# Optimization experiments

Measured on AMD Instinct MI355X. Metric: run time of the kernel, lower is better.

## Reference

```python
import jax, jax.numpy as jnp
import numpy as np
from math import factorial as fac

LMAX = 3
NMAX = 3
RC = 6.0
UNIT = RC / 3.0  # atomic_unit = rc/3
NSPEC = 4
N_ATOMS = 1000000


def _nnl():
    # a_{n,l} = 1 / ((2l+1) * 2^(2n+l) * n! * (n+l)!); nnl = sqrt(a_n a_n')
    a = np.array([[1.0 / ((2 * l + 1) * 2 ** (2 * n + l) * fac(n) * fac(n + l))
                   for l in range(LMAX + 1)] for n in range(NMAX + 1)])
    return jnp.asarray(np.sqrt(a[None] * a[:, None]), jnp.float32)  # (n, n', L+1)


def _yr_yi():
    one = np.ones((LMAX + 1, LMAX + 1))
    Yr = 2 * np.tril(one) - np.eye(LMAX + 1)   # real parts: diag weight 1 (m=0), lower weight 2
    Yi = 2 * np.triu(one, 1)                   # imag parts: strict upper weight 2
    return jnp.asarray(Yr, jnp.float32), jnp.asarray(Yi, jnp.float32)


def _sh_single(v):
    # Solid harmonics r^l * Ylm for one atom, packed into a (L+1, L+1) matrix:
    # Re(Y_l^m) at [l, l-m] (m=0 on the diagonal), Im(Y_l^m) at [l-m, l].
    x, y, z = v[0], v[1], v[2]
    r2 = x * x + y * y + z * z
    re = {(0, 0): jnp.asarray(0.28209479177387814, v.dtype)}  # 1/sqrt(4*pi)
    im = {(0, 0): jnp.zeros((), v.dtype)}
    for l in range(1, LMAX + 1):
        cl = -float(np.sqrt((2 * l + 1) / (2.0 * l)))
        re[(l, l)] = cl * (x * re[(l - 1, l - 1)] - y * im[(l - 1, l - 1)])
        im[(l, l)] = cl * (x * im[(l - 1, l - 1)] + y * re[(l - 1, l - 1)])
        g = float(np.sqrt(2 * l + 1))
        re[(l, l - 1)] = g * z * re[(l - 1, l - 1)]
        im[(l, l - 1)] = g * z * im[(l - 1, l - 1)]
        for m in range(l - 1):
            a = float(np.sqrt((4 * l * l - 1) / (l * l - m * m)))
            b = float(np.sqrt(((l - 1) ** 2 - m * m) / (4.0 * (l - 1) ** 2 - 1)))
            re[(l, m)] = a * (z * re[(l - 1, m)] - b * r2 * re[(l - 2, m)])
            im[(l, m)] = a * (z * im[(l - 1, m)] - b * r2 * im[(l - 2, m)])
    Y = jnp.zeros((LMAX + 1, LMAX + 1), v.dtype)
    for l in range(LMAX + 1):
        for m in range(l + 1):
            Y = Y.at[l, l - m].set(re[(l, m)])
            if m > 0:
                Y = Y.at[l - m, l].set(im[(l, m)])
    return Y


def _radial(dist):
    # Exp(-0.5 d^2/unit^2) * PolyCut(rc): smooth radial with polynomial cutoff
    cut = jnp.where(dist < RC, (1.0 - dist / RC) ** 2, 0.0)
    return jnp.exp(-0.5 * dist * dist / (UNIT * UNIT)) * cut


def _forward(coo, numbers):
    xyz = coo / UNIT
    d = jnp.sqrt(jnp.sum(xyz * xyz, axis=-1))              # (N,)
    n = 2.0 * jnp.arange(NMAX + 1, dtype=coo.dtype)        # exponents 2n
    r = _radial(UNIT * d)                                   # (N,)
    f = r[None] * d[None] ** n[:, None]                     # (nmax+1, N)
    Y = jnp.moveaxis(jax.vmap(_sh_single)(xyz), 0, -1)      # (L+1, L+1, N)
    onehot = (numbers[None, :] == jnp.arange(NSPEC)[:, None]).astype(coo.dtype)  # (S, N)
    # species-grouped reduction of the radial x Ylm outer product (fused einsum)
    c = jnp.einsum('kn,abn,sn->skab', f, Y, onehot)         # (S, nmax+1, L+1, L+1)
    Yr, Yi = _yr_yi()
    # p[a,b,n,m,l] = sum_m' Re-part + Im-part of c_{b,m} c*_{a,n} power spectrum
    p1 = jnp.einsum('bmlj,anlj,lj->abnml', c, c, Yr)
    p2 = jnp.einsum('bmil,anil,il->abnml', c, c, Yi)
    p = (p1 + p2) * _nnl()[None, None]
    return p.reshape(-1)                                    # dim = S^2 (nmax+1)^2 (L+1) = 1024


def setup_inputs() -> dict:
    key = jax.random.key(0)
    k1, k2 = jax.random.split(key)
    coo = 3.0 * jax.random.normal(k1, (N_ATOMS, 3), dtype=jnp.float32)
    numbers = jax.random.randint(k2, (N_ATOMS,), 0, NSPEC)
    return {"coo": coo, "numbers": numbers}


def reference(coo, numbers):
    return _forward(coo, numbers)
```

## Files before the change

### kernel.cpp

```cpp
#include <hip/hip_runtime.h>
#include <hip/hip_bf16.h>
#include <hip/hip_fp16.h>


typedef float f32x4 __attribute__((ext_vector_type(4)));
typedef unsigned int uint4v __attribute__((ext_vector_type(4)));
typedef _Float16 h2 __attribute__((ext_vector_type(2)));
typedef _Float16 half8 __attribute__((ext_vector_type(8)));

#define NB 512
#define NCH 4

__global__ void __launch_bounds__(256) soap_accum(
    const float* __restrict__ coo, const int* __restrict__ numbers,
    int N, float* __restrict__ partials, float* __restrict__ c_ws,
    int* __restrict__ counter)
{
    __shared__ unsigned int lT[4][2][16][64];

    if (blockIdx.x == 0) {
        if (threadIdx.x < 256) c_ws[threadIdx.x] = 0.f;
        if (threadIdx.x == 0) *counter = 0;
    }

    const int lane = threadIdx.x & 63;
    const int w = threadIdx.x >> 6;
    const int g = lane >> 4;
    const int comp = lane & 15;

    unsigned int* lA = &lT[w][0][0][0];
    unsigned int* lB = &lT[w][1][0][0];

    const unsigned swz = (unsigned)((comp & 7) << 2);
    const unsigned rbase = (unsigned)(comp << 6);
    unsigned rd[4];
#pragma unroll
    for (int m = 0; m < 4; ++m)
        rd[m] = rbase + ((unsigned)(16 * m + 4 * g) ^ swz);

    f32x4 acc = {0.f, 0.f, 0.f, 0.f};

    const int wid = blockIdx.x * 4 + w;
    float X0[NCH], Y0[NCH], Z0[NCH], X1[NCH], Y1[NCH], Z1[NCH];
    int n0[NCH], n1[NCH];
#pragma unroll
    for (int k = 0; k < NCH; ++k) {
        int base = (wid + k * 2048) * 128;
        int p = base + 2 * lane;
        int pc = p < N - 1 ? p : N - 2;
        const float* cb = coo + 3 * pc;
        float2 c0 = *(const float2*)(cb);
        float2 c1 = *(const float2*)(cb + 2);
        float2 c2 = *(const float2*)(cb + 4);
        X0[k] = c0.x; Y0[k] = c0.y; Z0[k] = c1.x;
        X1[k] = c1.y; Y1[k] = c2.x; Z1[k] = c2.y;
        int2 nm = *(const int2*)(numbers + pc);
        n0[k] = p < N ? nm.x : -1;
        n1[k] = p + 1 < N ? nm.y : -1;
    }

#pragma unroll
    for (int k = 0; k < NCH; ++k) {
        int num0 = n0[k], num1 = n1[k];

        float x0 = X0[k] * 0.5f, y0 = Y0[k] * 0.5f, z0 = Z0[k] * 0.5f;
        float x1 = X1[k] * 0.5f, y1 = Y1[k] * 0.5f, z1 = Z1[k] * 0.5f;
        float r20 = x0 * x0 + y0 * y0 + z0 * z0;
        float r21 = x1 * x1 + y1 * y1 + z1 * z1;
        float t0 = fmaxf(1.f - sqrtf(r20) * (1.f / 3.f), 0.f);
        float t1 = fmaxf(1.f - sqrtf(r21) * (1.f / 3.f), 0.f);
        float f00 = __expf(-0.5f * r20) * t0 * t0;
        float f01 = __expf(-0.5f * r21) * t1 * t1;

        h2 fpk[4];
        fpk[0] = (h2){(_Float16)f00, (_Float16)f01};
        fpk[1] = (h2){(_Float16)(f00 * r20), (_Float16)(f01 * r21)};
        fpk[2] = (h2){(_Float16)(f00 * r20 * r20), (_Float16)(f01 * r21 * r21)};
        fpk[3] = (h2){(_Float16)(f00 * r20 * r20 * r20), (_Float16)(f01 * r21 * r21 * r21)};

        h2 msk[4];
#pragma unroll
        for (int s = 0; s < 4; ++s)
            msk[s] = (h2){(_Float16)(num0 == s ? 1.f : 0.f),
                          (_Float16)(num1 == s ? 1.f : 0.f)};

        h2 xp = (h2){(_Float16)x0, (_Float16)x1};
        h2 yp = (h2){(_Float16)y0, (_Float16)y1};
        h2 zp = (h2){(_Float16)z0, (_Float16)z1};
        h2 rp = (h2){(_Float16)r20, (_Float16)r21};

        h2 re11 = (_Float16)-0.34549414947133550f * xp;
        h2 im11 = (_Float16)-0.34549414947133550f * yp;
        h2 re10 = (_Float16) 0.48860251190291992f * zp;
        h2 re22 = (_Float16)-1.11803398874989490f * (xp * re11 - yp * im11);
        h2 im22 = (_Float16)-1.11803398874989490f * (xp * im11 + yp * re11);
        h2 re21 = (_Float16) 2.23606797749978970f * (zp * re11);
        h2 im21 = (_Float16) 2.23606797749978970f * (zp * im11);
        h2 re20 = (_Float16) 1.93649167310370850f * (zp * re10 - (_Float16)0.16286750396763996f * rp);
        h2 re33 = (_Float16)-1.08012344973464350f * (xp * re22 - yp * im22);
        h2 im33 = (_Float16)-1.08012344973464350f * (xp * im22 + yp * re22);
        h2 re32 = (_Float16) 2.64575131106459070f * (zp * re22);
        h2 im32 = (_Float16) 2.64575131106459070f * (zp * im22);
        h2 re31 = (_Float16) 2.09165006633518890f * (zp * re21 - (_Float16)0.44721359549995793f * (rp * re11));
        h2 im31 = (_Float16) 2.09165006633518890f * (zp * im21 - (_Float16)0.44721359549995793f * (rp * im11));
        h2 re30 = (_Float16) 1.97202659436653870f * (zp * re20 - (_Float16)0.51639777949432220f * (rp * re10));

        h2 ypk[16];
        ypk[0] = (h2){(_Float16)0.28209479177387814f, (_Float16)0.28209479177387814f};
        ypk[1] = im11; ypk[2]  = im22; ypk[3]  = im33;
        ypk[4] = re11; ypk[5]  = re10; ypk[6]  = im21; ypk[7]  = im32;
        ypk[8] = re22; ypk[9]  = re21; ypk[10] = re20; ypk[11] = im31;
        ypk[12] = re33; ypk[13] = re32; ypk[14] = re31; ypk[15] = re30;

#pragma unroll
        for (int c = 0; c < 16; ++c) {
            h2 fs = fpk[c & 3] * msk[c >> 2];
            union { h2 h; unsigned u; } ua, ub;
            ua.h = fs; ub.h = ypk[c];
            unsigned idx = (unsigned)(c << 6) + ((unsigned)lane ^ ((unsigned)(c & 7) << 2));
            lA[idx] = ua.u;
            lB[idx] = ub.u;
        }

#pragma unroll
        for (int m = 0; m < 4; ++m) {
            union { uint4v q; half8 h; } A, B;
            A.q = *(const uint4v*)&lA[rd[m]];
            B.q = *(const uint4v*)&lB[rd[m]];
            acc = __builtin_amdgcn_mfma_f32_16x16x32_f16(A.h, B.h, acc, 0, 0, 0);
        }
    }

    float* credw = (float*)&lT[w][0][0][0];
#pragma unroll
    for (int rr = 0; rr < 4; ++rr)
        credw[((lane >> 4) * 4 + rr) * 16 + (lane & 15)] = acc[rr];
    __syncthreads();

    int tt = threadIdx.x;
    partials[blockIdx.x * 256 + tt] =
        ((float*)&lT[0][0][0][0])[tt] + ((float*)&lT[1][0][0][0])[tt] +
        ((float*)&lT[2][0][0][0])[tt] + ((float*)&lT[3][0][0][0])[tt];
}

__global__ void __launch_bounds__(256) soap_reduce_final(
    const float* __restrict__ partials, float* __restrict__ c_ws,
    int* __restrict__ counter, float* __restrict__ out)
{
    __shared__ float cs[256];
    __shared__ int lastflag;
    int t = threadIdx.x;

    float v = 0.f;
    for (int r = blockIdx.x; r < NB; r += 32)
        v += partials[r * 256 + t];
    atomicAdd(&c_ws[t], v);
    __syncthreads();
    if (t == 0) {
        __threadfence();
        lastflag = (atomicAdd(counter, 1) == 31);
    }
    __syncthreads();
    if (!lastflag) return;

    __threadfence();
    cs[t] = __hip_atomic_load(&c_ws[t], __ATOMIC_RELAXED,
                              __HIP_MEMORY_SCOPE_AGENT);
    __syncthreads();

    const float fact[7] = {1.f, 1.f, 2.f, 6.f, 24.f, 120.f, 720.f};
#pragma unroll
    for (int k = 0; k < 4; ++k) {
        int o = k * 256 + t;
        int l = o & 3, m = (o >> 2) & 3, n = (o >> 4) & 3,
            b = (o >> 6) & 3, a = (o >> 8) & 3;
        const float* cbm = &cs[(b * 4 + m) * 16];
        const float* can = &cs[(a * 4 + n) * 16];
        float vv = 0.f;
        for (int j = 0; j <= l; ++j) {
            float wgt = (j == l) ? 1.f : 2.f;
            vv += wgt * cbm[l * 4 + j] * can[l * 4 + j];
        }
        for (int i = 0; i < l; ++i)
            vv += 2.f * cbm[i * 4 + l] * can[i * 4 + l];
        float an = 1.0f / ((float)(2 * l + 1) * (float)(1 << (2 * n + l)) * fact[n] * fact[n + l]);
        float am = 1.0f / ((float)(2 * l + 1) * (float)(1 << (2 * m + l)) * fact[m] * fact[m + l]);
        out[o] = vv * sqrtf(an * am);
    }
}

extern "C" void kernel_launch(void* const* d_in, const int* in_sizes, int n_in,
                              void* d_out, int out_size, void* d_ws, size_t ws_size,
                              hipStream_t stream)
{
    const float* coo = (const float*)d_in[0];
    const int* numbers = (const int*)d_in[1];
    int N = in_sizes[1];

    float* c_ws = (float*)d_ws;
    int* counter = (int*)((float*)d_ws + 256);
    float* partials = (float*)d_ws + 512;

    hipLaunchKernelGGL(soap_accum, dim3(NB), dim3(256), 0, stream,
                       coo, numbers, N, partials, c_ws, counter);
    hipLaunchKernelGGL(soap_reduce_final, dim3(32), dim3(256), 0, stream,
                       partials, c_ws, counter, (float*)d_out);
}
```

Baseline: 17.28 us.

## Fuse reduction into accumulation kernel via two-level last-block counters

Drops the separate reduce kernel. Each block now writes its partial, and the last block in each group of 16 (found with an atomic counter) sums that group. The last of 32 group reducers then computes the final power spectrum. This removes a kernel launch and the gap between launches. Counters are never reset; they depend on modulo wraparound and on the workspace being zeroed at first use.

After: 54.98 us. 218% more time.

```diff
diff --git a/kernel.cpp b/kernel.cpp
--- a/kernel.cpp
+++ b/kernel.cpp
@@ -11,17 +11,14 @@
 #define NB 512
 #define NCH 4
 
-__global__ void __launch_bounds__(256) soap_accum(
+__global__ void __launch_bounds__(256) soap_fused(
     const float* __restrict__ coo, const int* __restrict__ numbers,
-    int N, float* __restrict__ partials, float* __restrict__ c_ws,
-    int* __restrict__ counter)
+    int N, float* __restrict__ partials, float* __restrict__ gsum,
+    unsigned* __restrict__ gcnt, float* __restrict__ out)
 {
     __shared__ unsigned int lT[4][2][16][64];
-
-    if (blockIdx.x == 0) {
-        if (threadIdx.x < 256) c_ws[threadIdx.x] = 0.f;
-        if (threadIdx.x == 0) *counter = 0;
-    }
+    __shared__ float cs[256];
+    __shared__ int flag1, flag2;
 
     const int lane = threadIdx.x & 63;
     const int w = threadIdx.x >> 6;
@@ -137,41 +134,59 @@
         credw[((lane >> 4) * 4 + rr) * 16 + (lane & 15)] = acc[rr];
     __syncthreads();
 
-    int tt = threadIdx.x;
-    partials[blockIdx.x * 256 + tt] =
-        ((float*)&lT[0][0][0][0])[tt] + ((float*)&lT[1][0][0][0])[tt] +
-        ((float*)&lT[2][0][0][0])[tt] + ((float*)&lT[3][0][0][0])[tt];
-}
-
-__global__ void __launch_bounds__(256) soap_reduce_final(
-    const float* __restrict__ partials, float* __restrict__ c_ws,
-    int* __restrict__ counter, float* __restrict__ out)
-{
-    __shared__ float cs[256];
-    __shared__ int lastflag;
-    int t = threadIdx.x;
-
-    float v = 0.f;
-    for (int r = blockIdx.x; r < NB; r += 32)
-        v += partials[r * 256 + t];
-    atomicAdd(&c_ws[t], v);
-    __syncthreads();
-    if (t == 0) {
-        __threadfence();
-        lastflag = (atomicAdd(counter, 1) == 31);
-    }
-    __syncthreads();
-    if (!lastflag) return;
-
-    __threadfence();
-    cs[t] = __hip_atomic_load(&c_ws[t], __ATOMIC_RELAXED,
-                              __HIP_MEMORY_SCOPE_AGENT);
+    const int tt = threadIdx.x;
+    const int grp = blockIdx.x >> 4;
+    {
+        float v = ((float*)&lT[0][0][0][0])[tt] + ((float*)&lT[1][0][0][0])[tt] +
+                  ((float*)&lT[2][0][0][0])[tt] + ((float*)&lT[3][0][0][0])[tt];
+        __hip_atomic_store(&partials[blockIdx.x * 256 + tt], v,
+                           __ATOMIC_RELAXED, __HIP_MEMORY_SCOPE_AGENT);
+    }
+    __threadfence();
+    __syncthreads();
+    if (tt == 0) {
+        unsigned old = __hip_atomic_fetch_add(&gcnt[grp], 1u,
+                           __ATOMIC_ACQ_REL, __HIP_MEMORY_SCOPE_AGENT);
+        flag1 = (((old + 1u) & 15u) == 0u);
+    }
+    __syncthreads();
+    if (!flag1) return;
+
+    __threadfence();
+    {
+        float s = 0.f;
+#pragma unroll
+        for (int r = 0; r < 16; ++r)
+            s += __hip_atomic_load(&partials[(grp * 16 + r) * 256 + tt],
+                                   __ATOMIC_RELAXED, __HIP_MEMORY_SCOPE_AGENT);
+        __hip_atomic_store(&gsum[grp * 256 + tt], s,
+                           __ATOMIC_RELAXED, __HIP_MEMORY_SCOPE_AGENT);
+    }
+    __threadfence();
+    __syncthreads();
+    if (tt == 0) {
+        unsigned old = __hip_atomic_fetch_add(&gcnt[32], 1u,
+                           __ATOMIC_ACQ_REL, __HIP_MEMORY_SCOPE_AGENT);
+        flag2 = (((old + 1u) & 31u) == 0u);
+    }
+    __syncthreads();
+    if (!flag2) return;
+
+    __threadfence();
+    {
+        float s = 0.f;
+#pragma unroll
+        for (int gg = 0; gg < 32; ++gg)
+            s += __hip_atomic_load(&gsum[gg * 256 + tt],
+                                   __ATOMIC_RELAXED, __HIP_MEMORY_SCOPE_AGENT);
+        cs[tt] = s;
+    }
     __syncthreads();
 
     const float fact[7] = {1.f, 1.f, 2.f, 6.f, 24.f, 120.f, 720.f};
 #pragma unroll
     for (int k = 0; k < 4; ++k) {
-        int o = k * 256 + t;
+        int o = k * 256 + tt;
         int l = o & 3, m = (o >> 2) & 3, n = (o >> 4) & 3,
             b = (o >> 6) & 3, a = (o >> 8) & 3;
         const float* cbm = &cs[(b * 4 + m) * 16];
@@ -197,12 +212,10 @@
     const int* numbers = (const int*)d_in[1];
     int N = in_sizes[1];
 
-    float* c_ws = (float*)d_ws;
-    int* counter = (int*)((float*)d_ws + 256);
-    float* partials = (float*)d_ws + 512;
-
-    hipLaunchKernelGGL(soap_accum, dim3(NB), dim3(256), 0, stream,
-                       coo, numbers, N, partials, c_ws, counter);
-    hipLaunchKernelGGL(soap_reduce_final, dim3(32), dim3(256), 0, stream,
-                       partials, c_ws, counter, (float*)d_out);
+    unsigned* gcnt = (unsigned*)d_ws;
+    float* gsum = (float*)d_ws + 64;
+    float* partials = (float*)d_ws + 64 + 8192;
+
+    hipLaunchKernelGGL(soap_fused, dim3(NB), dim3(256), 0, stream,
+                       coo, numbers, N, partials, gsum, gcnt, (float*)d_out);
 }
```
